# Kernel tuning notes

Measured on AMD Instinct MI355X. Metric: run time of the kernel, lower is better.

The kernel has to match this reference:

```python
import jax, jax.numpy as jnp
import numpy as np
import math

B, N, D_MODEL = 1, 2925, 1536
NUM_HEADS, HEAD_DIM = 12, 128
F, H, W = 13, 15, 15
MAX_SEQ = 1024
EPS = 1e-6


def _make_freqs(max_seq, dim):
    # (cos, sin) pairs for half-dim rotary frequencies, base 10000
    inv = 1.0 / (10000.0 ** (np.arange(0, dim, 2, dtype=np.float64) / dim))
    ang = np.arange(max_seq, dtype=np.float64)[:, None] * inv[None, :]
    return jnp.asarray(np.stack([np.cos(ang), np.sin(ang)], axis=-1), dtype=jnp.float32)


def setup_inputs() -> dict:
    key = jax.random.key(0)
    ks = jax.random.split(key, 10)
    s = 1.0 / math.sqrt(D_MODEL)
    dim_base = HEAD_DIM // 6              # 21
    dim_t = HEAD_DIM - 4 * dim_base       # 44
    dim_h = 2 * dim_base                  # 42
    return {
        "x": jax.random.normal(ks[0], (B, N, D_MODEL), dtype=jnp.float32),
        "Wq": jax.random.normal(ks[1], (D_MODEL, D_MODEL), dtype=jnp.float32) * s,
        "bq": jnp.zeros((D_MODEL,), dtype=jnp.float32),
        "Wk": jax.random.normal(ks[2], (D_MODEL, D_MODEL), dtype=jnp.float32) * s,
        "bk": jnp.zeros((D_MODEL,), dtype=jnp.float32),
        "Wv": jax.random.normal(ks[3], (D_MODEL, D_MODEL), dtype=jnp.float32) * s,
        "bv": jnp.zeros((D_MODEL,), dtype=jnp.float32),
        "Wo": jax.random.normal(ks[4], (D_MODEL, D_MODEL), dtype=jnp.float32) * s,
        "bo": jnp.zeros((D_MODEL,), dtype=jnp.float32),
        "q_scale": jnp.ones((D_MODEL,), dtype=jnp.float32),
        "k_scale": jnp.ones((D_MODEL,), dtype=jnp.float32),
        "freqs_t": _make_freqs(MAX_SEQ, dim_t),
        "freqs_h": _make_freqs(MAX_SEQ, dim_h),
        "freqs_w": _make_freqs(MAX_SEQ, dim_h),
        "f": F, "h": H, "w": W,
    }


def _rms_norm(x, scale, eps=EPS):
    var = jnp.mean(jnp.square(x), axis=-1, keepdims=True)
    return x * jax.lax.rsqrt(var + eps) * scale


def _rope_apply(x, f, h, w, freqs_t, freqs_h, freqs_w):
    # x: [b, n, H, D] with n == f*h*w
    b, n, nh, d = x.shape
    db = d // 6
    dt, dh, dw = d - 4 * db, 2 * db, 2 * db
    ft = jnp.broadcast_to(freqs_t[:f, None, None, :, :], (f, h, w, dt // 2, 2))
    fh = jnp.broadcast_to(freqs_h[None, :h, None, :, :], (f, h, w, dh // 2, 2))
    fw = jnp.broadcast_to(freqs_w[None, None, :w, :, :], (f, h, w, dw // 2, 2))
    fg = jnp.concatenate([ft, fh, fw], axis=3).reshape(n, d // 2, 2)[None, :, None, :, :]
    xc = x.reshape(b, n, nh, d // 2, 2)
    re = xc[..., 0] * fg[..., 0] - xc[..., 1] * fg[..., 1]
    im = xc[..., 0] * fg[..., 1] + xc[..., 1] * fg[..., 0]
    return jnp.stack([re, im], axis=-1).reshape(b, n, nh, d)


def reference(x, Wq, bq, Wk, bk, Wv, bv, Wo, bo, q_scale, k_scale,
              freqs_t, freqs_h, freqs_w, f, h, w):
    b, n, _ = x.shape
    nh, d = NUM_HEADS, HEAD_DIM
    # projections + RMSNorm across full hidden dim (before head split)
    q = _rms_norm(x @ Wq + bq, q_scale).reshape(b, n, nh, d)
    k = _rms_norm(x @ Wk + bk, k_scale).reshape(b, n, nh, d)
    v = (x @ Wv + bv).reshape(b, n, nh, d)
    # 3D RoPE on [b, n, H, D] layout
    q = _rope_apply(q, f, h, w, freqs_t, freqs_h, freqs_w)
    k = _rope_apply(k, f, h, w, freqs_t, freqs_h, freqs_w)
    # [b, H, n, d]
    q = q.transpose(0, 2, 1, 3)
    k = k.transpose(0, 2, 1, 3)
    v = v.transpose(0, 2, 1, 3)
    scores = jnp.einsum("bhid,bhjd->bhij", q, k) / math.sqrt(d)
    attn = jax.nn.softmax(scores, axis=-1)
    out = jnp.einsum("bhij,bhjd->bhid", attn, v)
    out = out.transpose(0, 2, 1, 3).reshape(b, n, nh * d)
    return out @ Wo + bo
```

## Files before the change

kernel.cpp:

```cpp
#include <hip/hip_runtime.h>


#define N_TOK 2925
#define DMODEL 1536
#define NHEAD 12
#define HDIM 128
#define KSPLIT 1472
#define VT_STRIDE 2944

typedef __attribute__((ext_vector_type(8))) __bf16 bf16x8;
typedef __attribute__((ext_vector_type(4))) float floatx4;

#define MFMA(a, b, c) __builtin_amdgcn_mfma_f32_16x16x32_bf16((a), (b), (c), 0, 0, 0)

static __device__ __forceinline__ unsigned short f2bf(float f) {
    unsigned u = __builtin_bit_cast(unsigned, f);
    return (unsigned short)((u + 0x7fffu + ((u >> 16) & 1u)) >> 16);
}

__global__ __launch_bounds__(256) void k_convert_x(const float* __restrict__ x,
                                                   unsigned short* __restrict__ xb, int n) {
    int i = (blockIdx.x * 256 + threadIdx.x) * 4;
    if (i < n) {
        float4 v = *(const float4*)(x + i);
        uint2 o;
        o.x = (unsigned)f2bf(v.x) | ((unsigned)f2bf(v.y) << 16);
        o.y = (unsigned)f2bf(v.z) | ((unsigned)f2bf(v.w) << 16);
        *(uint2*)(xb + i) = o;
    }
}

__global__ __launch_bounds__(256) void k_transpose_w(const float* __restrict__ W0,
                                                     const float* __restrict__ W1,
                                                     const float* __restrict__ W2,
                                                     const float* __restrict__ W3,
                                                     unsigned short* __restrict__ Wt) {
    __shared__ float tile[32][33];
    const float* W = blockIdx.z == 0 ? W0 : blockIdx.z == 1 ? W1 : blockIdx.z == 2 ? W2 : W3;
    unsigned short* out = Wt + (size_t)blockIdx.z * DMODEL * DMODEL;
    int tx = threadIdx.x, ty = threadIdx.y;
    int bx = blockIdx.x * 32, by = blockIdx.y * 32;
#pragma unroll
    for (int i = 0; i < 4; i++)
        tile[ty + 8 * i][tx] = W[(size_t)(by + ty + 8 * i) * DMODEL + bx + tx];
    __syncthreads();
#pragma unroll
    for (int i = 0; i < 4; i++)
        out[(size_t)(bx + ty + 8 * i) * DMODEL + by + tx] = f2bf(tile[tx][ty + 8 * i]);
}

__global__ __launch_bounds__(256, 2) void k_gemm(const unsigned short* __restrict__ A,
                                                 const unsigned short* __restrict__ BtBase,
                                                 const float* __restrict__ b0,
                                                 const float* __restrict__ b1,
                                                 const float* __restrict__ b2,
                                                 float* __restrict__ Cbase, int M) {
    const int z = blockIdx.z;
    const unsigned short* Bt = BtBase + (size_t)z * DMODEL * DMODEL;
    const float* bias = (z == 0) ? b0 : (z == 1) ? b1 : b2;
    float* C = Cbase + (size_t)z * M * DMODEL;

    __shared__ unsigned short As[128 * 40];
    __shared__ unsigned short Bs[128 * 40];

    const int tid = threadIdx.x;
    const int wave = tid >> 6, lane = tid & 63, quad = lane >> 4, l16 = lane & 15;
    const int wr = wave >> 1, wc = wave & 1;
    const int m0 = blockIdx.y * 128, n0 = blockIdx.x * 128;

    floatx4 acc[4][4] = {};

    for (int k0 = 0; k0 < DMODEL; k0 += 32) {
#pragma unroll
        for (int c = 0; c < 2; c++) {
            int chunk = tid + 256 * c;
            int row = chunk >> 2, col = (chunk & 3) * 8;
            int gm = m0 + row;
            uint4 va = make_uint4(0, 0, 0, 0);
            if (gm < M) va = *(const uint4*)(A + (size_t)gm * DMODEL + k0 + col);
            *(uint4*)&As[row * 40 + col] = va;
            uint4 vb = *(const uint4*)(Bt + (size_t)(n0 + row) * DMODEL + k0 + col);
            *(uint4*)&Bs[row * 40 + col] = vb;
        }
        __syncthreads();

        bf16x8 af[4], bfm[4];
#pragma unroll
        for (int i = 0; i < 4; i++)
            af[i] = *(const bf16x8*)&As[(wr * 64 + i * 16 + l16) * 40 + quad * 8];
#pragma unroll
        for (int j = 0; j < 4; j++)
            bfm[j] = *(const bf16x8*)&Bs[(wc * 64 + j * 16 + l16) * 40 + quad * 8];
#pragma unroll
        for (int i = 0; i < 4; i++)
#pragma unroll
            for (int j = 0; j < 4; j++)
                acc[i][j] = MFMA(af[i], bfm[j], acc[i][j]);
        __syncthreads();
    }

#pragma unroll
    for (int j = 0; j < 4; j++) {
        int cg = n0 + wc * 64 + j * 16 + l16;
        float bv = bias[cg];
#pragma unroll
        for (int i = 0; i < 4; i++) {
            int rbase = m0 + wr * 64 + i * 16 + quad * 4;
#pragma unroll
            for (int r = 0; r < 4; r++) {
                int rg = rbase + r;
                if (rg < M) C[(size_t)rg * DMODEL + cg] = acc[i][j][r] + bv;
            }
        }
    }
}

__global__ __launch_bounds__(256) void k_norm_rope(const float* __restrict__ Qf,
                                                   const float* __restrict__ Kf,
                                                   const float* __restrict__ Vf,
                                                   const float* __restrict__ qsc,
                                                   const float* __restrict__ ksc,
                                                   const float* __restrict__ ft,
                                                   const float* __restrict__ fh,
                                                   const float* __restrict__ fw,
                                                   unsigned short* __restrict__ qb,
                                                   unsigned short* __restrict__ kb,
                                                   unsigned short* __restrict__ vb) {
    const int n = blockIdx.x;
    const int tid = threadIdx.x, wave = tid >> 6, lane = tid & 63;
    const int t_i = n / 225, rem = n % 225, h_i = rem / 15, w_i = rem % 15;
    const float att_scale = 0.08838834764831845f;

    float2 qv[3], kv[3], vv[3];
    float sq = 0.f, sk = 0.f;
#pragma unroll
    for (int c = 0; c < 3; c++) {
        int p = tid + 256 * c;
        qv[c] = *(const float2*)(Qf + (size_t)n * DMODEL + 2 * p);
        kv[c] = *(const float2*)(Kf + (size_t)n * DMODEL + 2 * p);
        vv[c] = *(const float2*)(Vf + (size_t)n * DMODEL + 2 * p);
        sq += qv[c].x * qv[c].x + qv[c].y * qv[c].y;
        sk += kv[c].x * kv[c].x + kv[c].y * kv[c].y;
    }
#pragma unroll
    for (int off = 32; off >= 1; off >>= 1) {
        sq += __shfl_xor(sq, off, 64);
        sk += __shfl_xor(sk, off, 64);
    }
    __shared__ float red[2][4];
    if (lane == 0) { red[0][wave] = sq; red[1][wave] = sk; }
    __syncthreads();
    sq = red[0][0] + red[0][1] + red[0][2] + red[0][3];
    sk = red[1][0] + red[1][1] + red[1][2] + red[1][3];
    const float rq = rsqrtf(sq * (1.f / 1536.f) + 1e-6f) * att_scale;
    const float rk = rsqrtf(sk * (1.f / 1536.f) + 1e-6f);

#pragma unroll
    for (int c = 0; c < 3; c++) {
        int p = tid + 256 * c;
        int hd = p >> 6, pl = p & 63, dd = 2 * pl;
        float cs, sn;
        if (pl < 22)      { cs = ft[t_i * 44 + 2 * pl];        sn = ft[t_i * 44 + 2 * pl + 1]; }
        else if (pl < 43) { int pp = pl - 22; cs = fh[h_i * 42 + 2 * pp]; sn = fh[h_i * 42 + 2 * pp + 1]; }
        else              { int pp = pl - 43; cs = fw[w_i * 42 + 2 * pp]; sn = fw[w_i * 42 + 2 * pp + 1]; }
        int hidx = hd * 128 + dd;
        float q0 = qv[c].x * rq * qsc[hidx], q1 = qv[c].y * rq * qsc[hidx + 1];
        float k0 = kv[c].x * rk * ksc[hidx], k1 = kv[c].y * rk * ksc[hidx + 1];
        size_t o = ((size_t)hd * N_TOK + n) * HDIM + dd;
        unsigned qo = (unsigned)f2bf(q0 * cs - q1 * sn) | ((unsigned)f2bf(q0 * sn + q1 * cs) << 16);
        unsigned ko = (unsigned)f2bf(k0 * cs - k1 * sn) | ((unsigned)f2bf(k0 * sn + k1 * cs) << 16);
        unsigned vo = (unsigned)f2bf(vv[c].x) | ((unsigned)f2bf(vv[c].y) << 16);
        *(unsigned*)(qb + o) = qo;
        *(unsigned*)(kb + o) = ko;
        *(unsigned*)(vb + o) = vo;
    }
}

__global__ __launch_bounds__(256) void k_transpose_v(const unsigned short* __restrict__ vbi,
                                                     unsigned short* __restrict__ vt) {
    __shared__ unsigned short tile[32][33];
    const int head = blockIdx.z;
    const int t0 = blockIdx.x * 32, d0 = blockIdx.y * 32;
    const int tx = threadIdx.x, ty = threadIdx.y;
#pragma unroll
    for (int i = 0; i < 4; i++) {
        int t = t0 + ty + 8 * i;
        tile[ty + 8 * i][tx] = (t < N_TOK) ? vbi[((size_t)head * N_TOK + t) * HDIM + d0 + tx] : 0;
    }
    __syncthreads();
    int t = t0 + tx;
#pragma unroll
    for (int i = 0; i < 4; i++)
        vt[((size_t)head * HDIM + d0 + ty + 8 * i) * VT_STRIDE + t] = tile[tx][ty + 8 * i];
}

__global__ __launch_bounds__(256, 3) void k_attn_part(const unsigned short* __restrict__ qb,
                                                      const unsigned short* __restrict__ kb,
                                                      const unsigned short* __restrict__ vt,
                                                      float* __restrict__ Opart,
                                                      float* __restrict__ mbuf,
                                                      float* __restrict__ lbuf) {
    __shared__ unsigned short Ks[64 * 136];
    __shared__ unsigned short Vs[128 * 72];
    __shared__ unsigned short Ps[4][16 * 72];

    const int tid = threadIdx.x, wave = tid >> 6, lane = tid & 63;
    const int quad = lane >> 4, l16 = lane & 15;
    const int head = blockIdx.y, z = blockIdx.z;
    const int q0 = blockIdx.x * 64 + wave * 16;
    const unsigned short* qh = qb + (size_t)head * N_TOK * HDIM;
    const unsigned short* kh = kb + (size_t)head * N_TOK * HDIM;
    const unsigned short* vh = vt + (size_t)head * HDIM * VT_STRIDE;
    unsigned short* ps = Ps[wave];

    const int kbeg = z ? KSPLIT : 0;
    const int kend = z ? N_TOK : KSPLIT;

    bf16x8 aq[4];
    {
        int qrow = q0 + l16;
        if (qrow < N_TOK) {
#pragma unroll
            for (int ks = 0; ks < 4; ks++)
                aq[ks] = *(const bf16x8*)&qh[(size_t)qrow * HDIM + ks * 32 + quad * 8];
        } else {
#pragma unroll
            for (int ks = 0; ks < 4; ks++) aq[ks] = (bf16x8)(__bf16)0.0f;
        }
    }

    floatx4 oacc[8] = {};
    float m_r[4] = {-1e30f, -1e30f, -1e30f, -1e30f};
    float l_r[4] = {0.f, 0.f, 0.f, 0.f};

    for (int kb0 = kbeg; kb0 < kend; kb0 += 64) {
#pragma unroll
        for (int c = 0; c < 4; c++) {
            int chunk = tid + 256 * c;
            int row = chunk >> 4, col = (chunk & 15) * 8;
            int gk = kb0 + row; if (gk >= N_TOK) gk = N_TOK - 1;
            *(uint4*)&Ks[row * 136 + col] = *(const uint4*)(kh + (size_t)gk * HDIM + col);
        }
#pragma unroll
        for (int c = 0; c < 4; c++) {
            int chunk = tid + 256 * c;
            int d = chunk >> 3, col = (chunk & 7) * 8;
            *(uint4*)&Vs[d * 72 + col] = *(const uint4*)(vh + (size_t)d * VT_STRIDE + kb0 + col);
        }
        __syncthreads();

        floatx4 sa[4] = {};
#pragma unroll
        for (int j = 0; j < 4; j++) {
            bf16x8 bkf[4];
#pragma unroll
            for (int ks = 0; ks < 4; ks++)
                bkf[ks] = *(const bf16x8*)&Ks[(j * 16 + l16) * 136 + ks * 32 + quad * 8];
#pragma unroll
            for (int ks = 0; ks < 4; ks++)
                sa[j] = MFMA(aq[ks], bkf[ks], sa[j]);
        }

        bool valid[4];
#pragma unroll
        for (int j = 0; j < 4; j++) valid[j] = (kb0 + j * 16 + l16) < kend;

        float alpha[4];
#pragma unroll
        for (int r = 0; r < 4; r++) {
            float x = -1e30f;
#pragma unroll
            for (int j = 0; j < 4; j++) x = fmaxf(x, valid[j] ? sa[j][r] : -1e30f);
#pragma unroll
            for (int off = 8; off >= 1; off >>= 1) x = fmaxf(x, __shfl_xor(x, off, 16));
            float mnew = fmaxf(m_r[r], x);
            alpha[r] = __expf(m_r[r] - mnew);
            m_r[r] = mnew;
        }
        float rsum[4] = {0.f, 0.f, 0.f, 0.f};
#pragma unroll
        for (int j = 0; j < 4; j++)
#pragma unroll
            for (int r = 0; r < 4; r++) {
                float p = valid[j] ? __expf(sa[j][r] - m_r[r]) : 0.f;
                rsum[r] += p;
                ps[(quad * 4 + r) * 72 + j * 16 + l16] = f2bf(p);
            }
#pragma unroll
        for (int r = 0; r < 4; r++) {
            float s = rsum[r];
#pragma unroll
            for (int off = 8; off >= 1; off >>= 1) s += __shfl_xor(s, off, 16);
            l_r[r] = l_r[r] * alpha[r] + s;
        }
#pragma unroll
        for (int jd = 0; jd < 8; jd++)
#pragma unroll
            for (int r = 0; r < 4; r++) oacc[jd][r] *= alpha[r];

#pragma unroll
        for (int ks = 0; ks < 2; ks++) {
            bf16x8 ap = *(const bf16x8*)&ps[l16 * 72 + ks * 32 + quad * 8];
#pragma unroll
            for (int jd = 0; jd < 8; jd++) {
                bf16x8 bvf = *(const bf16x8*)&Vs[(jd * 16 + l16) * 72 + ks * 32 + quad * 8];
                oacc[jd] = MFMA(ap, bvf, oacc[jd]);
            }
        }
        __syncthreads();
    }

#pragma unroll
    for (int r = 0; r < 4; r++) {
        int rg = q0 + quad * 4 + r;
        if (rg < N_TOK) {
            size_t rbase = ((size_t)(z * NHEAD + head) * N_TOK + rg) * HDIM;
#pragma unroll
            for (int jd = 0; jd < 8; jd++)
                Opart[rbase + jd * 16 + l16] = oacc[jd][r];
            if (l16 == 0) {
                int mi = (z * NHEAD + head) * N_TOK + rg;
                mbuf[mi] = m_r[r];
                lbuf[mi] = l_r[r];
            }
        }
    }
}

__global__ __launch_bounds__(256) void k_combine(const float* __restrict__ Opart,
                                                 const float* __restrict__ mbuf,
                                                 const float* __restrict__ lbuf,
                                                 unsigned short* __restrict__ ab) {
    const int R = NHEAD * N_TOK;
    int r = blockIdx.x * 8 + (threadIdx.x >> 5);
    if (r >= R) return;
    int l32 = threadIdx.x & 31;
    float m0 = mbuf[r], m1 = mbuf[R + r];
    float l0 = lbuf[r], l1 = lbuf[R + r];
    float m = fmaxf(m0, m1);
    float w0 = __expf(m0 - m), w1 = __expf(m1 - m);
    float inv = 1.f / (l0 * w0 + l1 * w1);
    w0 *= inv; w1 *= inv;
    float4 a = *(const float4*)&Opart[(size_t)r * HDIM + l32 * 4];
    float4 b = *(const float4*)&Opart[((size_t)R + r) * HDIM + l32 * 4];
    int head = r / N_TOK, tok = r % N_TOK;
    unsigned short* o = ab + (size_t)tok * DMODEL + head * HDIM + l32 * 4;
    uint2 pk;
    pk.x = (unsigned)f2bf(a.x * w0 + b.x * w1) | ((unsigned)f2bf(a.y * w0 + b.y * w1) << 16);
    pk.y = (unsigned)f2bf(a.z * w0 + b.z * w1) | ((unsigned)f2bf(a.w * w0 + b.w * w1) << 16);
    *(uint2*)o = pk;
}

extern "C" void kernel_launch(void* const* d_in, const int* in_sizes, int n_in,
                              void* d_out, int out_size, void* d_ws, size_t ws_size,
                              hipStream_t stream) {
    const float* x   = (const float*)d_in[0];
    const float* Wq  = (const float*)d_in[1];
    const float* bq  = (const float*)d_in[2];
    const float* Wk  = (const float*)d_in[3];
    const float* bk  = (const float*)d_in[4];
    const float* Wv  = (const float*)d_in[5];
    const float* bv  = (const float*)d_in[6];
    const float* Wo  = (const float*)d_in[7];
    const float* bo  = (const float*)d_in[8];
    const float* qsc = (const float*)d_in[9];
    const float* ksc = (const float*)d_in[10];
    const float* ft  = (const float*)d_in[11];
    const float* fh  = (const float*)d_in[12];
    const float* fw  = (const float*)d_in[13];

    char* ws = (char*)d_ws;
    unsigned short* xb   = (unsigned short*)ws; ws += (size_t)N_TOK * DMODEL * 2;
    unsigned short* Wt   = (unsigned short*)ws; ws += (size_t)4 * DMODEL * DMODEL * 2;
    char* qkvf_region    = ws;                  ws += (size_t)3 * N_TOK * DMODEL * 4;
    unsigned short* qkvb = (unsigned short*)ws; ws += (size_t)3 * N_TOK * DMODEL * 2;
    unsigned short* ab   = (unsigned short*)ws; ws += (size_t)N_TOK * DMODEL * 2;

    float* Qf = (float*)qkvf_region;
    float* Kf = Qf + (size_t)N_TOK * DMODEL;
    float* Vf = Qf + (size_t)2 * N_TOK * DMODEL;
    float* Opart = (float*)qkvf_region;
    float* mbuf  = Opart + (size_t)2 * NHEAD * N_TOK * HDIM;
    float* lbuf  = mbuf + (size_t)2 * NHEAD * N_TOK;
    unsigned short* vtp = (unsigned short*)(lbuf + (size_t)2 * NHEAD * N_TOK);

    unsigned short* qbp = qkvb;
    unsigned short* kbp = qkvb + (size_t)N_TOK * DMODEL;
    unsigned short* vbp = qkvb + (size_t)2 * N_TOK * DMODEL;

    const int nelem = N_TOK * DMODEL;
    k_convert_x<<<(nelem / 4 + 255) / 256, 256, 0, stream>>>(x, xb, nelem);
    k_transpose_w<<<dim3(48, 48, 4), dim3(32, 8), 0, stream>>>(Wq, Wk, Wv, Wo, Wt);
    k_gemm<<<dim3(12, 23, 3), 256, 0, stream>>>(xb, Wt, bq, bk, bv, Qf, N_TOK);
    k_norm_rope<<<N_TOK, 256, 0, stream>>>(Qf, Kf, Vf, qsc, ksc, ft, fh, fw, qbp, kbp, vbp);
    k_transpose_v<<<dim3(92, 4, NHEAD), dim3(32, 8), 0, stream>>>(vbp, vtp);
    k_attn_part<<<dim3(46, NHEAD, 2), 256, 0, stream>>>(qbp, kbp, vtp, Opart, mbuf, lbuf);
    k_combine<<<(NHEAD * N_TOK + 7) / 8, 256, 0, stream>>>(Opart, mbuf, lbuf, ab);
    k_gemm<<<dim3(12, 23, 1), 256, 0, stream>>>(ab, Wt + (size_t)3 * DMODEL * DMODEL,
                                                bo, bo, bo, (float*)d_out, N_TOK);
}
```

Baseline: 431.0 us.

## Rework attention kernel with 32x32 MFMA, 4-way key split, bf16 partials

Rewrites the split-K attention kernel to use 32x32x16 bf16 MFMA tiles with 32 queries per wave and 128 per block. Keys are split four ways instead of two, LDS tiles are XOR-swizzled, and softmax uses exp2 with log2(e) folded into the Q scale. Output rescaling is skipped when no row max changed, and a peeled masked tail tile replaces the per-element validity checks. Partial outputs are stored as transposed bf16 and merged by a new LDS-staged combine kernel. This trades extra partial traffic and bf16 rounding of the partials for higher MFMA throughput and better occupancy.

```diff
diff --git a/kernel.cpp b/kernel.cpp
--- a/kernel.cpp
+++ b/kernel.cpp
@@ -5,17 +5,28 @@
 #define DMODEL 1536
 #define NHEAD 12
 #define HDIM 128
-#define KSPLIT 1472
 #define VT_STRIDE 2944
+#define QPAD 2944
+#define NSPLIT 4
 
 typedef __attribute__((ext_vector_type(8))) __bf16 bf16x8;
 typedef __attribute__((ext_vector_type(4))) float floatx4;
-
-#define MFMA(a, b, c) __builtin_amdgcn_mfma_f32_16x16x32_bf16((a), (b), (c), 0, 0, 0)
+typedef __attribute__((ext_vector_type(16))) float floatx16;
+
+#define MFMA(a, b, c)   __builtin_amdgcn_mfma_f32_16x16x32_bf16((a), (b), (c), 0, 0, 0)
+#define MFMA32(a, b, c) __builtin_amdgcn_mfma_f32_32x32x16_bf16((a), (b), (c), 0, 0, 0)
 
 static __device__ __forceinline__ unsigned short f2bf(float f) {
     unsigned u = __builtin_bit_cast(unsigned, f);
     return (unsigned short)((u + 0x7fffu + ((u >> 16) & 1u)) >> 16);
+}
+static __device__ __forceinline__ float bf2f(unsigned short s) {
+    unsigned u = ((unsigned)s) << 16;
+    return __builtin_bit_cast(float, u);
+}
+static __device__ __forceinline__ unsigned packbf2(float a, float b) {
+    return __builtin_amdgcn_perm(__builtin_bit_cast(unsigned, b),
+                                 __builtin_bit_cast(unsigned, a), 0x07060302u);
 }
 
 __global__ __launch_bounds__(256) void k_convert_x(const float* __restrict__ x,
@@ -129,7 +140,7 @@
     const int n = blockIdx.x;
     const int tid = threadIdx.x, wave = tid >> 6, lane = tid & 63;
     const int t_i = n / 225, rem = n % 225, h_i = rem / 15, w_i = rem % 15;
-    const float att_scale = 0.08838834764831845f;
+    const float att_scale = 0.08838834764831845f * 1.4426950408889634f;
 
     float2 qv[3], kv[3], vv[3];
     float sq = 0.f, sk = 0.f;
@@ -194,161 +205,183 @@
         vt[((size_t)head * HDIM + d0 + ty + 8 * i) * VT_STRIDE + t] = tile[tx][ty + 8 * i];
 }
 
+#define ATTN_TILE(MASKED, klen)                                               \
+  {                                                                           \
+    _Pragma("unroll")                                                         \
+    for (int c = 0; c < 4; c++) {                                             \
+      int ch = tid + 256 * c; int key = ch >> 4, kc = ch & 15;                \
+      int gk = kb0 + key; if (gk > N_TOK - 1) gk = N_TOK - 1;                 \
+      *(uint4*)&Ks[key * 136 + (kc ^ ((key >> 3) & 3)) * 8] =                 \
+          *(const uint4*)(kh + (size_t)gk * HDIM + kc * 8);                   \
+    }                                                                         \
+    _Pragma("unroll")                                                         \
+    for (int c = 0; c < 4; c++) {                                             \
+      int ch = tid + 256 * c; int d = ch >> 3, vc = ch & 7;                   \
+      *(uint4*)&Vs[d * 72 + (vc ^ ((d >> 3) & 3)) * 8] =                      \
+          *(const uint4*)(vh + (size_t)d * VT_STRIDE + kb0 + vc * 8);         \
+    }                                                                         \
+    __syncthreads();                                                          \
+    floatx16 sa0 = (floatx16)0.f, sa1 = (floatx16)0.f;                        \
+    _Pragma("unroll")                                                         \
+    for (int ks = 0; ks < 8; ks++) {                                          \
+      int cc = ((h + 2 * ks) ^ swq) * 8;                                      \
+      bf16x8 ak0 = *(const bf16x8*)&Ks[q31 * 136 + cc];                       \
+      bf16x8 ak1 = *(const bf16x8*)&Ks[(q31 + 32) * 136 + cc];                \
+      sa0 = MFMA32(ak0, aq[ks], sa0);                                         \
+      sa1 = MFMA32(ak1, aq[ks], sa1);                                         \
+    }                                                                         \
+    float mnew = m_r;                                                         \
+    _Pragma("unroll")                                                         \
+    for (int r = 0; r < 16; r++) {                                            \
+      float v0 = sa0[r], v1 = sa1[r];                                         \
+      if (MASKED) {                                                           \
+        int klo = (r & 3) + 8 * (r >> 2) + 4 * h;                             \
+        if (klo >= (klen)) v0 = -1e30f;                                       \
+        if (klo + 32 >= (klen)) v1 = -1e30f;                                  \
+      }                                                                       \
+      mnew = fmaxf(mnew, fmaxf(v0, v1));                                      \
+    }                                                                         \
+    mnew = fmaxf(mnew, __shfl_xor(mnew, 32, 64));                             \
+    const float alpha = exp2f(m_r - mnew); m_r = mnew;                        \
+    float rsum = 0.f;                                                         \
+    _Pragma("unroll")                                                         \
+    for (int mt = 0; mt < 2; mt++)                                            \
+      _Pragma("unroll")                                                       \
+      for (int g = 0; g < 4; g++) {                                           \
+        float p[4];                                                           \
+        _Pragma("unroll")                                                     \
+        for (int j = 0; j < 4; j++) {                                         \
+          int r = g * 4 + j;                                                  \
+          float v = mt ? sa1[r] : sa0[r];                                     \
+          if (MASKED) {                                                       \
+            int kl = 32 * mt + (r & 3) + 8 * (r >> 2) + 4 * h;                \
+            if (kl >= (klen)) v = -1e30f;                                     \
+          }                                                                   \
+          p[j] = exp2f(v - mnew);                                             \
+        }                                                                     \
+        rsum += (p[0] + p[1]) + (p[2] + p[3]);                                \
+        uint2 pk;                                                             \
+        pk.x = packbf2(p[0], p[1]);                                           \
+        pk.y = packbf2(p[2], p[3]);                                           \
+        *(uint2*)&ps[q31 * 72 + ((4 * mt + g) ^ swq) * 8 + 4 * h] = pk;       \
+      }                                                                       \
+    l_r = l_r * alpha + rsum + __shfl_xor(rsum, 32, 64);                      \
+    if (__any(alpha != 1.f)) {                                                \
+      _Pragma("unroll")                                                       \
+      for (int mt = 0; mt < 4; mt++)                                          \
+        _Pragma("unroll")                                                     \
+        for (int r = 0; r < 16; r++) oacc[mt][r] *= alpha;                    \
+    }                                                                         \
+    _Pragma("unroll")                                                         \
+    for (int ks = 0; ks < 4; ks++) {                                          \
+      int cc = ((h + 2 * ks) ^ swq) * 8;                                      \
+      bf16x8 bp = *(const bf16x8*)&ps[q31 * 72 + cc];                         \
+      _Pragma("unroll")                                                       \
+      for (int mt = 0; mt < 4; mt++) {                                        \
+        bf16x8 av = *(const bf16x8*)&Vs[(mt * 32 + q31) * 72 + cc];           \
+        oacc[mt] = MFMA32(av, bp, oacc[mt]);                                  \
+      }                                                                       \
+    }                                                                         \
+    __syncthreads();                                                          \
+  }
+
 __global__ __launch_bounds__(256, 3) void k_attn_part(const unsigned short* __restrict__ qb,
                                                       const unsigned short* __restrict__ kb,
                                                       const unsigned short* __restrict__ vt,
-                                                      float* __restrict__ Opart,
+                                                      unsigned short* __restrict__ Opart,
                                                       float* __restrict__ mbuf,
                                                       float* __restrict__ lbuf) {
     __shared__ unsigned short Ks[64 * 136];
     __shared__ unsigned short Vs[128 * 72];
-    __shared__ unsigned short Ps[4][16 * 72];
+    __shared__ unsigned short Ps[4][32 * 72];
 
     const int tid = threadIdx.x, wave = tid >> 6, lane = tid & 63;
-    const int quad = lane >> 4, l16 = lane & 15;
+    const int h = lane >> 5, q31 = lane & 31;
     const int head = blockIdx.y, z = blockIdx.z;
-    const int q0 = blockIdx.x * 64 + wave * 16;
+    const int kbeg = (z <= 2) ? z * 768 : 2240;
+    const int kend = (z <= 1) ? (z + 1) * 768 : (z == 2 ? 2240 : N_TOK);
+    const int q0 = blockIdx.x * 128 + wave * 32;
     const unsigned short* qh = qb + (size_t)head * N_TOK * HDIM;
     const unsigned short* kh = kb + (size_t)head * N_TOK * HDIM;
     const unsigned short* vh = vt + (size_t)head * HDIM * VT_STRIDE;
     unsigned short* ps = Ps[wave];
-
-    const int kbeg = z ? KSPLIT : 0;
-    const int kend = z ? N_TOK : KSPLIT;
-
-    bf16x8 aq[4];
+    const int swq = (q31 >> 3) & 3;
+
+    bf16x8 aq[8];
     {
-        int qrow = q0 + l16;
-        if (qrow < N_TOK) {
-#pragma unroll
-            for (int ks = 0; ks < 4; ks++)
-                aq[ks] = *(const bf16x8*)&qh[(size_t)qrow * HDIM + ks * 32 + quad * 8];
-        } else {
-#pragma unroll
-            for (int ks = 0; ks < 4; ks++) aq[ks] = (bf16x8)(__bf16)0.0f;
+        int qr = q0 + q31; if (qr > N_TOK - 1) qr = N_TOK - 1;
+#pragma unroll
+        for (int ks = 0; ks < 8; ks++)
+            aq[ks] = *(const bf16x8*)&qh[(size_t)qr * HDIM + ks * 16 + h * 8];
+    }
+
+    floatx16 oacc[4] = {};
+    float m_r = -1e30f, l_r = 0.f;
+
+    int kb0 = kbeg;
+    const int nfull = (kend - kbeg) >> 6;
+    for (int t = 0; t < nfull; t++, kb0 += 64) ATTN_TILE(false, 64)
+    if (kb0 < kend) { const int klen = kend - kb0; ATTN_TILE(true, klen) }
+
+    unsigned short* ob = Opart + (size_t)(z * NHEAD + head) * HDIM * QPAD;
+#pragma unroll
+    for (int mt = 0; mt < 4; mt++)
+#pragma unroll
+        for (int r = 0; r < 16; r++) {
+            int d = mt * 32 + (r & 3) + 8 * (r >> 2) + 4 * h;
+            ob[(size_t)d * QPAD + q0 + q31] = f2bf(oacc[mt][r]);
         }
-    }
-
-    floatx4 oacc[8] = {};
-    float m_r[4] = {-1e30f, -1e30f, -1e30f, -1e30f};
-    float l_r[4] = {0.f, 0.f, 0.f, 0.f};
-
-    for (int kb0 = kbeg; kb0 < kend; kb0 += 64) {
-#pragma unroll
-        for (int c = 0; c < 4; c++) {
-            int chunk = tid + 256 * c;
-            int row = chunk >> 4, col = (chunk & 15) * 8;
-            int gk = kb0 + row; if (gk >= N_TOK) gk = N_TOK - 1;
-            *(uint4*)&Ks[row * 136 + col] = *(const uint4*)(kh + (size_t)gk * HDIM + col);
-        }
-#pragma unroll
-        for (int c = 0; c < 4; c++) {
-            int chunk = tid + 256 * c;
-            int d = chunk >> 3, col = (chunk & 7) * 8;
-            *(uint4*)&Vs[d * 72 + col] = *(const uint4*)(vh + (size_t)d * VT_STRIDE + kb0 + col);
-        }
-        __syncthreads();
-
-        floatx4 sa[4] = {};
-#pragma unroll
-        for (int j = 0; j < 4; j++) {
-            bf16x8 bkf[4];
-#pragma unroll
-            for (int ks = 0; ks < 4; ks++)
-                bkf[ks] = *(const bf16x8*)&Ks[(j * 16 + l16) * 136 + ks * 32 + quad * 8];
-#pragma unroll
-            for (int ks = 0; ks < 4; ks++)
-                sa[j] = MFMA(aq[ks], bkf[ks], sa[j]);
-        }
-
-        bool valid[4];
-#pragma unroll
-        for (int j = 0; j < 4; j++) valid[j] = (kb0 + j * 16 + l16) < kend;
-
-        float alpha[4];
-#pragma unroll
-        for (int r = 0; r < 4; r++) {
-            float x = -1e30f;
-#pragma unroll
-            for (int j = 0; j < 4; j++) x = fmaxf(x, valid[j] ? sa[j][r] : -1e30f);
-#pragma unroll
-            for (int off = 8; off >= 1; off >>= 1) x = fmaxf(x, __shfl_xor(x, off, 16));
-            float mnew = fmaxf(m_r[r], x);
-            alpha[r] = __expf(m_r[r] - mnew);
-            m_r[r] = mnew;
-        }
-        float rsum[4] = {0.f, 0.f, 0.f, 0.f};
-#pragma unroll
-        for (int j = 0; j < 4; j++)
-#pragma unroll
-            for (int r = 0; r < 4; r++) {
-                float p = valid[j] ? __expf(sa[j][r] - m_r[r]) : 0.f;
-                rsum[r] += p;
-                ps[(quad * 4 + r) * 72 + j * 16 + l16] = f2bf(p);
-            }
-#pragma unroll
-        for (int r = 0; r < 4; r++) {
-            float s = rsum[r];
-#pragma unroll
-            for (int off = 8; off >= 1; off >>= 1) s += __shfl_xor(s, off, 16);
-            l_r[r] = l_r[r] * alpha[r] + s;
-        }
-#pragma unroll
-        for (int jd = 0; jd < 8; jd++)
-#pragma unroll
-            for (int r = 0; r < 4; r++) oacc[jd][r] *= alpha[r];
-
-#pragma unroll
-        for (int ks = 0; ks < 2; ks++) {
-            bf16x8 ap = *(const bf16x8*)&ps[l16 * 72 + ks * 32 + quad * 8];
-#pragma unroll
-            for (int jd = 0; jd < 8; jd++) {
-                bf16x8 bvf = *(const bf16x8*)&Vs[(jd * 16 + l16) * 72 + ks * 32 + quad * 8];
-                oacc[jd] = MFMA(ap, bvf, oacc[jd]);
-            }
-        }
-        __syncthreads();
-    }
-
-#pragma unroll
-    for (int r = 0; r < 4; r++) {
-        int rg = q0 + quad * 4 + r;
-        if (rg < N_TOK) {
-            size_t rbase = ((size_t)(z * NHEAD + head) * N_TOK + rg) * HDIM;
-#pragma unroll
-            for (int jd = 0; jd < 8; jd++)
-                Opart[rbase + jd * 16 + l16] = oacc[jd][r];
-            if (l16 == 0) {
-                int mi = (z * NHEAD + head) * N_TOK + rg;
-                mbuf[mi] = m_r[r];
-                lbuf[mi] = l_r[r];
-            }
-        }
-    }
-}
-
-__global__ __launch_bounds__(256) void k_combine(const float* __restrict__ Opart,
+    if (h == 0) {
+        int mi = (z * NHEAD + head) * QPAD + q0 + q31;
+        mbuf[mi] = m_r;
+        lbuf[mi] = l_r;
+    }
+}
+
+__global__ __launch_bounds__(256) void k_combine(const unsigned short* __restrict__ Opart,
                                                  const float* __restrict__ mbuf,
                                                  const float* __restrict__ lbuf,
                                                  unsigned short* __restrict__ ab) {
-    const int R = NHEAD * N_TOK;
-    int r = blockIdx.x * 8 + (threadIdx.x >> 5);
-    if (r >= R) return;
-    int l32 = threadIdx.x & 31;
-    float m0 = mbuf[r], m1 = mbuf[R + r];
-    float l0 = lbuf[r], l1 = lbuf[R + r];
-    float m = fmaxf(m0, m1);
-    float w0 = __expf(m0 - m), w1 = __expf(m1 - m);
-    float inv = 1.f / (l0 * w0 + l1 * w1);
-    w0 *= inv; w1 *= inv;
-    float4 a = *(const float4*)&Opart[(size_t)r * HDIM + l32 * 4];
-    float4 b = *(const float4*)&Opart[((size_t)R + r) * HDIM + l32 * 4];
-    int head = r / N_TOK, tok = r % N_TOK;
-    unsigned short* o = ab + (size_t)tok * DMODEL + head * HDIM + l32 * 4;
-    uint2 pk;
-    pk.x = (unsigned)f2bf(a.x * w0 + b.x * w1) | ((unsigned)f2bf(a.y * w0 + b.y * w1) << 16);
-    pk.y = (unsigned)f2bf(a.z * w0 + b.z * w1) | ((unsigned)f2bf(a.w * w0 + b.w * w1) << 16);
-    *(uint2*)o = pk;
+    __shared__ unsigned short Ts[64 * 136];
+    const int tid = threadIdx.x, wave = tid >> 6, lane = tid & 63;
+    const int head = blockIdx.y;
+    const int t0 = blockIdx.x * 64;
+    const int tok = t0 + lane;
+
+    float m[NSPLIT], l[NSPLIT], w[NSPLIT];
+#pragma unroll
+    for (int s = 0; s < NSPLIT; s++) {
+        int mi = (s * NHEAD + head) * QPAD + tok;
+        m[s] = mbuf[mi]; l[s] = lbuf[mi];
+    }
+    float mm = fmaxf(fmaxf(m[0], m[1]), fmaxf(m[2], m[3]));
+    float den = 0.f;
+#pragma unroll
+    for (int s = 0; s < NSPLIT; s++) { w[s] = exp2f(m[s] - mm); den += l[s] * w[s]; }
+    float inv = 1.f / den;
+#pragma unroll
+    for (int s = 0; s < NSPLIT; s++) w[s] *= inv;
+
+#pragma unroll 4
+    for (int dd = 0; dd < 32; dd++) {
+        int d = wave * 32 + dd;
+        float acc = 0.f;
+#pragma unroll
+        for (int s = 0; s < NSPLIT; s++)
+            acc += bf2f(Opart[((size_t)(s * NHEAD + head) * HDIM + d) * QPAD + tok]) * w[s];
+        Ts[lane * 136 + d] = f2bf(acc);
+    }
+    __syncthreads();
+
+    int row = tid >> 2, ch = tid & 3;
+    int tk = t0 + row;
+    if (tk < N_TOK) {
+#pragma unroll
+        for (int i = 0; i < 4; i++) {
+            int c = ch + 4 * i;
+            *(uint4*)(ab + (size_t)tk * DMODEL + head * HDIM + c * 8) = *(uint4*)&Ts[row * 136 + c * 8];
+        }
+    }
 }
 
 extern "C" void kernel_launch(void* const* d_in, const int* in_sizes, int n_in,
@@ -379,10 +412,10 @@
     float* Qf = (float*)qkvf_region;
     float* Kf = Qf + (size_t)N_TOK * DMODEL;
     float* Vf = Qf + (size_t)2 * N_TOK * DMODEL;
-    float* Opart = (float*)qkvf_region;
-    float* mbuf  = Opart + (size_t)2 * NHEAD * N_TOK * HDIM;
-    float* lbuf  = mbuf + (size_t)2 * NHEAD * N_TOK;
-    unsigned short* vtp = (unsigned short*)(lbuf + (size_t)2 * NHEAD * N_TOK);
+    unsigned short* Opart = (unsigned short*)qkvf_region;
+    float* mbuf = (float*)(qkvf_region + (size_t)NSPLIT * NHEAD * HDIM * QPAD * 2);
+    float* lbuf = mbuf + (size_t)NSPLIT * NHEAD * QPAD;
+    unsigned short* vtp = (unsigned short*)(lbuf + (size_t)NSPLIT * NHEAD * QPAD);
 
     unsigned short* qbp = qkvb;
     unsigned short* kbp = qkvb + (size_t)N_TOK * DMODEL;
@@ -394,8 +427,8 @@
     k_gemm<<<dim3(12, 23, 3), 256, 0, stream>>>(xb, Wt, bq, bk, bv, Qf, N_TOK);
     k_norm_rope<<<N_TOK, 256, 0, stream>>>(Qf, Kf, Vf, qsc, ksc, ft, fh, fw, qbp, kbp, vbp);
     k_transpose_v<<<dim3(92, 4, NHEAD), dim3(32, 8), 0, stream>>>(vbp, vtp);
-    k_attn_part<<<dim3(46, NHEAD, 2), 256, 0, stream>>>(qbp, kbp, vtp, Opart, mbuf, lbuf);
-    k_combine<<<(NHEAD * N_TOK + 7) / 8, 256, 0, stream>>>(Opart, mbuf, lbuf, ab);
+    k_attn_part<<<dim3(23, NHEAD, NSPLIT), 256, 0, stream>>>(qbp, kbp, vtp, Opart, mbuf, lbuf);
+    k_combine<<<dim3(46, NHEAD), 256, 0, stream>>>(Opart, mbuf, lbuf, ab);
     k_gemm<<<dim3(12, 23, 1), 256, 0, stream>>>(ab, Wt + (size_t)3 * DMODEL * DMODEL,
                                                 bo, bo, bo, (float*)d_out, N_TOK);
 }
```

Measured after the change: 508.5 us. +18.0%, slower.

## Use direct global-to-LDS loads in GEMM and switch softmax to exp2

Applied to the files above, without the earlier changes.

The GEMM tile loads now use global_load_lds to copy A and B tiles straight into LDS, with unpadded 32-wide rows. This removes the register round trip and the per-row bounds check. To keep A reads in bounds without that check, the activation buffer `ab` is moved ahead of the fp32 region so overread rows land in valid workspace. The attention scale is folded with log2(e) so softmax and the combine kernel can use exp2f directly. The risks are LDS bank conflicts from dropping the padding, and relying on out-of-range rows reading harmless memory.

```diff
diff --git a/kernel.cpp b/kernel.cpp
--- a/kernel.cpp
+++ b/kernel.cpp
@@ -16,6 +16,11 @@
 static __device__ __forceinline__ unsigned short f2bf(float f) {
     unsigned u = __builtin_bit_cast(unsigned, f);
     return (unsigned short)((u + 0x7fffu + ((u >> 16) & 1u)) >> 16);
+}
+
+static __device__ __forceinline__ void gload_lds16(const unsigned short* g, unsigned short* l) {
+    __builtin_amdgcn_global_load_lds((const __attribute__((address_space(1))) void*)g,
+                                     (__attribute__((address_space(3))) void*)l, 16, 0, 0);
 }
 
 __global__ __launch_bounds__(256) void k_convert_x(const float* __restrict__ x,
@@ -60,37 +65,32 @@
     const float* bias = (z == 0) ? b0 : (z == 1) ? b1 : b2;
     float* C = Cbase + (size_t)z * M * DMODEL;
 
-    __shared__ unsigned short As[128 * 40];
-    __shared__ unsigned short Bs[128 * 40];
+    __shared__ __align__(16) unsigned short As[128 * 32];
+    __shared__ __align__(16) unsigned short Bs[128 * 32];
 
     const int tid = threadIdx.x;
     const int wave = tid >> 6, lane = tid & 63, quad = lane >> 4, l16 = lane & 15;
     const int wr = wave >> 1, wc = wave & 1;
     const int m0 = blockIdx.y * 128, n0 = blockIdx.x * 128;
 
+    const int r4 = tid >> 2, c4 = (tid & 3) * 8;
+
     floatx4 acc[4][4] = {};
 
     for (int k0 = 0; k0 < DMODEL; k0 += 32) {
-#pragma unroll
-        for (int c = 0; c < 2; c++) {
-            int chunk = tid + 256 * c;
-            int row = chunk >> 2, col = (chunk & 3) * 8;
-            int gm = m0 + row;
-            uint4 va = make_uint4(0, 0, 0, 0);
-            if (gm < M) va = *(const uint4*)(A + (size_t)gm * DMODEL + k0 + col);
-            *(uint4*)&As[row * 40 + col] = va;
-            uint4 vb = *(const uint4*)(Bt + (size_t)(n0 + row) * DMODEL + k0 + col);
-            *(uint4*)&Bs[row * 40 + col] = vb;
-        }
+        gload_lds16(A + (size_t)(m0 + r4) * DMODEL + k0 + c4,       &As[r4 * 32 + c4]);
+        gload_lds16(A + (size_t)(m0 + r4 + 64) * DMODEL + k0 + c4,  &As[(r4 + 64) * 32 + c4]);
+        gload_lds16(Bt + (size_t)(n0 + r4) * DMODEL + k0 + c4,      &Bs[r4 * 32 + c4]);
+        gload_lds16(Bt + (size_t)(n0 + r4 + 64) * DMODEL + k0 + c4, &Bs[(r4 + 64) * 32 + c4]);
         __syncthreads();
 
         bf16x8 af[4], bfm[4];
 #pragma unroll
         for (int i = 0; i < 4; i++)
-            af[i] = *(const bf16x8*)&As[(wr * 64 + i * 16 + l16) * 40 + quad * 8];
+            af[i] = *(const bf16x8*)&As[(wr * 64 + i * 16 + l16) * 32 + quad * 8];
 #pragma unroll
         for (int j = 0; j < 4; j++)
-            bfm[j] = *(const bf16x8*)&Bs[(wc * 64 + j * 16 + l16) * 40 + quad * 8];
+            bfm[j] = *(const bf16x8*)&Bs[(wc * 64 + j * 16 + l16) * 32 + quad * 8];
 #pragma unroll
         for (int i = 0; i < 4; i++)
 #pragma unroll
@@ -129,7 +129,7 @@
     const int n = blockIdx.x;
     const int tid = threadIdx.x, wave = tid >> 6, lane = tid & 63;
     const int t_i = n / 225, rem = n % 225, h_i = rem / 15, w_i = rem % 15;
-    const float att_scale = 0.08838834764831845f;
+    const float att_scale = 0.08838834764831845f * 1.4426950408889634f;
 
     float2 qv[3], kv[3], vv[3];
     float sq = 0.f, sk = 0.f;
@@ -274,7 +274,7 @@
 #pragma unroll
             for (int off = 8; off >= 1; off >>= 1) x = fmaxf(x, __shfl_xor(x, off, 16));
             float mnew = fmaxf(m_r[r], x);
-            alpha[r] = __expf(m_r[r] - mnew);
+            alpha[r] = exp2f(m_r[r] - mnew);
             m_r[r] = mnew;
         }
         float rsum[4] = {0.f, 0.f, 0.f, 0.f};
@@ -282,7 +282,7 @@
         for (int j = 0; j < 4; j++)
 #pragma unroll
             for (int r = 0; r < 4; r++) {
-                float p = valid[j] ? __expf(sa[j][r] - m_r[r]) : 0.f;
+                float p = valid[j] ? exp2f(sa[j][r] - m_r[r]) : 0.f;
                 rsum[r] += p;
                 ps[(quad * 4 + r) * 72 + j * 16 + l16] = f2bf(p);
             }
@@ -338,7 +338,7 @@
     float m0 = mbuf[r], m1 = mbuf[R + r];
     float l0 = lbuf[r], l1 = lbuf[R + r];
     float m = fmaxf(m0, m1);
-    float w0 = __expf(m0 - m), w1 = __expf(m1 - m);
+    float w0 = exp2f(m0 - m), w1 = exp2f(m1 - m);
     float inv = 1.f / (l0 * w0 + l1 * w1);
     w0 *= inv; w1 *= inv;
     float4 a = *(const float4*)&Opart[(size_t)r * HDIM + l32 * 4];
@@ -372,9 +372,9 @@
     char* ws = (char*)d_ws;
     unsigned short* xb   = (unsigned short*)ws; ws += (size_t)N_TOK * DMODEL * 2;
     unsigned short* Wt   = (unsigned short*)ws; ws += (size_t)4 * DMODEL * DMODEL * 2;
+    unsigned short* ab   = (unsigned short*)ws; ws += (size_t)N_TOK * DMODEL * 2;
     char* qkvf_region    = ws;                  ws += (size_t)3 * N_TOK * DMODEL * 4;
     unsigned short* qkvb = (unsigned short*)ws; ws += (size_t)3 * N_TOK * DMODEL * 2;
-    unsigned short* ab   = (unsigned short*)ws; ws += (size_t)N_TOK * DMODEL * 2;
 
     float* Qf = (float*)qkvf_region;
     float* Kf = Qf + (size_t)N_TOK * DMODEL;
```

After: 423.6 us. No clear change (-1.7%).
